# Kernel tuning notes

Measured on AMD Instinct MI355X. Metric: run time of the kernel, lower is better.

Reference implementation:

```python
import jax, jax.numpy as jnp
import numpy as np

T, B, M, H, NH = 4, 8, 1024, 768, 12
HD = H // NH
KMAX = 10


def _ln(x, s, b):
    mu = x.mean(-1, keepdims=True)
    var = ((x - mu) ** 2).mean(-1, keepdims=True)
    return (x - mu) * jax.lax.rsqrt(var + 1e-5) * s + b


def setup_inputs() -> dict:
    key = jax.random.key(0)
    ks = jax.random.split(key, 10)
    init = lambda k, shp: jax.random.normal(k, shp, jnp.float32) * 0.02
    return {
        'x': jax.random.normal(ks[0], (B, M, H), jnp.float32),
        'overlap': jax.random.randint(ks[1], (B, M, M), 0, KMAX + 1, jnp.int32),
        'lp': -jax.random.uniform(ks[2], (B, M), jnp.float32) * 10.0,
        'ln1_s': jnp.ones((T, H)), 'ln1_b': jnp.zeros((T, H)),
        'Wqkv': init(ks[3], (T, H, 3 * H)),
        'Wout': init(ks[4], (T, H, H)), 'bout': jnp.zeros((T, H)),
        'ln2_s': jnp.ones((T, H)), 'ln2_b': jnp.zeros((T, H)),
        'W1': init(ks[5], (T, H, 4 * H)), 'b1': jnp.zeros((T, 4 * H)),
        'W2': init(ks[6], (T, 4 * H, H)), 'b2': jnp.zeros((T, H)),
        'lno_s': jnp.ones((H,)), 'lno_b': jnp.zeros((H,)),
        'ov_emb': init(ks[7], (KMAX + 1,)),
        'ht_alpha': jnp.ones((1,), jnp.float32),
    }


def reference(x, overlap, lp, ln1_s, ln1_b, Wqkv, Wout, bout, ln2_s, ln2_b,
              W1, b1, W2, b2, lno_s, lno_b, ov_emb, ht_alpha):
    lp_c = jnp.clip(lp, -30.0, 0.0)                      # [B,M]
    ov = ov_emb[jnp.minimum(overlap, KMAX)]              # [B,M,M]
    bias = (ov - ht_alpha[0] * lp_c[:, None, :])[:, None]  # [B,1,M,M]
    scale = 1.0 / jnp.sqrt(jnp.float32(HD))
    for t in range(T):
        r = _ln(x, ln1_s[t], ln1_b[t])
        q, k, v = jnp.split(r @ Wqkv[t], 3, axis=-1)
        q = q.reshape(B, M, NH, HD).transpose(0, 2, 1, 3)
        k = k.reshape(B, M, NH, HD).transpose(0, 2, 1, 3)
        v = v.reshape(B, M, NH, HD).transpose(0, 2, 1, 3)
        s = jnp.einsum('bhqd,bhkd->bhqk', q, k) * scale + bias
        a = jax.nn.softmax(s, axis=-1)
        o = jnp.einsum('bhqk,bhkd->bhqd', a, v).transpose(0, 2, 1, 3).reshape(B, M, H)
        x = x + o @ Wout[t] + bout[t]
        h = _ln(x, ln2_s[t], ln2_b[t])
        x = x + jax.nn.gelu(h @ W1[t] + b1[t], approximate=False) @ W2[t] + b2[t]
    x = _ln(x, lno_s, lno_b)
    w = jax.nn.softmax(-lp_c, axis=1)                    # HT weights over m tokens
    return jnp.einsum('bm,bmh->bh', w, x)
```

## Files before the change

### kernel.cpp

```cpp
#include <hip/hip_runtime.h>
#include <hip/hip_bf16.h>
#include <math.h>

#define TT 4
#define BB 8
#define MM 1024
#define HH 768
#define NHEAD 12
#define HDIM 64
#define NTOK 8192
#define H3 2304
#define H4 3072

typedef __attribute__((ext_vector_type(8))) short bf16x8;
typedef __attribute__((ext_vector_type(4))) float f32x4;
typedef __attribute__((ext_vector_type(4))) unsigned short u16x4;

#define GLOBAL_AS(p) ((const __attribute__((address_space(1))) void*)(p))
#define LDS_AS(p)    ((__attribute__((address_space(3))) void*)(p))

__device__ __forceinline__ unsigned short f2bf(float f) {
  union { float f; unsigned u; } v; v.f = f;
  unsigned r = v.u + 0x7fffu + ((v.u >> 16) & 1u);
  return (unsigned short)(r >> 16);
}

__device__ __forceinline__ float fast_exp2(float x) {
#if __has_builtin(__builtin_amdgcn_exp2f)
  return __builtin_amdgcn_exp2f(x);
#else
  return exp2f(x);
#endif
}

__device__ __forceinline__ f32x4 mfma16(bf16x8 a, bf16x8 b, f32x4 c) {
  return __builtin_amdgcn_mfma_f32_16x16x32_bf16(a, b, c, 0, 0, 0);
}

__device__ __forceinline__ float block_sum256(float v, float* sh) {
  #pragma unroll
  for (int off = 32; off > 0; off >>= 1) v += __shfl_down(v, off);
  if ((threadIdx.x & 63) == 0) sh[threadIdx.x >> 6] = v;
  __syncthreads();
  v = sh[0] + sh[1] + sh[2] + sh[3];
  __syncthreads();
  return v;
}

__device__ __forceinline__ float block_max256(float v, float* sh) {
  #pragma unroll
  for (int off = 32; off > 0; off >>= 1) v = fmaxf(v, __shfl_down(v, off));
  if ((threadIdx.x & 63) == 0) sh[threadIdx.x >> 6] = v;
  __syncthreads();
  v = fmaxf(fmaxf(sh[0], sh[1]), fmaxf(sh[2], sh[3]));
  __syncthreads();
  return v;
}

__global__ __launch_bounds__(256) void wconv_kernel(const float* __restrict__ W,
                                                    unsigned short* __restrict__ Wt,
                                                    int K, int N) {
  __shared__ float tile[32][33];
  const int n0 = blockIdx.x * 32, k0 = blockIdx.y * 32;
  const int tx = threadIdx.x, ty = threadIdx.y;
  #pragma unroll
  for (int j = 0; j < 4; j++)
    tile[ty + j*8][tx] = W[(size_t)(k0 + ty + j*8) * N + n0 + tx];
  __syncthreads();
  #pragma unroll
  for (int j = 0; j < 4; j++)
    Wt[(size_t)(n0 + ty + j*8) * K + k0 + tx] = f2bf(tile[tx][ty + j*8]);
}

__global__ __launch_bounds__(256) void ln_kernel(const float* __restrict__ x,
                                                 const float* __restrict__ s,
                                                 const float* __restrict__ b,
                                                 unsigned short* __restrict__ out) {
  __shared__ float sh[4];
  const int row = blockIdx.x;
  const int tid = threadIdx.x;
  const float* xr = x + (size_t)row * HH;
  float v[3];
  float sum = 0.f;
  #pragma unroll
  for (int j = 0; j < 3; j++) { v[j] = xr[tid + j*256]; sum += v[j]; }
  sum = block_sum256(sum, sh);
  const float mu = sum * (1.f/768.f);
  float ss = 0.f;
  #pragma unroll
  for (int j = 0; j < 3; j++) { float d = v[j] - mu; ss += d*d; }
  ss = block_sum256(ss, sh);
  const float rstd = rsqrtf(ss * (1.f/768.f) + 1e-5f);
  #pragma unroll
  for (int j = 0; j < 3; j++) {
    int col = tid + j*256;
    out[(size_t)row * HH + col] = f2bf((v[j]-mu)*rstd*s[col] + b[col]);
  }
}

template<int EPI>
__global__ __launch_bounds__(256) void gemm_kernel(const unsigned short* __restrict__ A,
                                                   const unsigned short* __restrict__ Bt,
                                                   unsigned short* __restrict__ outB,
                                                   float* __restrict__ outF,
                                                   const float* __restrict__ bias,
                                                   int Ng, int Kg, int nx) {
  __shared__ unsigned short a_lds[2][128*64];
  __shared__ unsigned short b_lds[2][128*64];
  const int tid = threadIdx.x;
  const int w = tid >> 6, l = tid & 63;
  const int nwg = gridDim.x;
  const int lin = blockIdx.x;
  const int L = (lin & 7) * (nwg >> 3) + (lin >> 3);
  const int m0 = (L / nx) * 128, n0 = (L % nx) * 128;

  const int wr = (w >> 1) * 64, wc = (w & 1) * 64;
  const int l15 = l & 15, lhi = l >> 4;
  const int srow = w*32 + (l >> 3);
  const int schunk = (l & 7) ^ (l >> 3);
  const int scol = schunk << 3;

  f32x4 acc[4][4] = {};
  const int nk = Kg >> 6;
  int cur = 0;

  #pragma unroll
  for (int i = 0; i < 4; i++) {
    const unsigned short* gsa = A  + (size_t)(m0 + srow + i*8)*Kg + scol;
    const unsigned short* gsb = Bt + (size_t)(n0 + srow + i*8)*Kg + scol;
    __builtin_amdgcn_global_load_lds(GLOBAL_AS(gsa), LDS_AS(&a_lds[0][w*2048 + i*512]), 16, 0, 0);
    __builtin_amdgcn_global_load_lds(GLOBAL_AS(gsb), LDS_AS(&b_lds[0][w*2048 + i*512]), 16, 0, 0);
  }
  __syncthreads();

  for (int t = 0; t < nk; t++) {
    if (t + 1 < nk) {
      const int ks = (t + 1) << 6;
      #pragma unroll
      for (int i = 0; i < 4; i++) {
        const unsigned short* gsa = A  + (size_t)(m0 + srow + i*8)*Kg + ks + scol;
        const unsigned short* gsb = Bt + (size_t)(n0 + srow + i*8)*Kg + ks + scol;
        __builtin_amdgcn_global_load_lds(GLOBAL_AS(gsa), LDS_AS(&a_lds[cur^1][w*2048 + i*512]), 16, 0, 0);
        __builtin_amdgcn_global_load_lds(GLOBAL_AS(gsb), LDS_AS(&b_lds[cur^1][w*2048 + i*512]), 16, 0, 0);
      }
    }
    const unsigned short* ab = &a_lds[cur][0];
    const unsigned short* bb = &b_lds[cur][0];
    #pragma unroll
    for (int kb = 0; kb < 2; kb++) {
      bf16x8 af[4], bfr[4];
      const int rc = (kb*4 + lhi) ^ (l15 & 7);
      #pragma unroll
      for (int rb = 0; rb < 4; rb++)
        af[rb] = *(const bf16x8*)&ab[(wr + rb*16 + l15)*64 + (rc << 3)];
      #pragma unroll
      for (int nb = 0; nb < 4; nb++)
        bfr[nb] = *(const bf16x8*)&bb[(wc + nb*16 + l15)*64 + (rc << 3)];
      #pragma unroll
      for (int rb = 0; rb < 4; rb++)
        #pragma unroll
        for (int nb = 0; nb < 4; nb++)
          acc[rb][nb] = mfma16(af[rb], bfr[nb], acc[rb][nb]);
    }
    __syncthreads();
    cur ^= 1;
  }

  const int lr = lhi << 2;
  #pragma unroll
  for (int rb = 0; rb < 4; rb++)
    #pragma unroll
    for (int nb = 0; nb < 4; nb++) {
      const int row = m0 + wr + rb*16 + lr;
      const int col = n0 + wc + nb*16 + l15;
      #pragma unroll
      for (int r = 0; r < 4; r++) {
        float v = acc[rb][nb][r];
        const size_t off = (size_t)(row + r)*Ng + col;
        if (EPI == 0) {
          outB[off] = f2bf(v);
        } else if (EPI == 1) {
          v += bias[col];
          float u = 0.79788456080287f * v * (1.f + 0.044715f * v * v);
          u = fminf(u, 15.f);
          float e = fast_exp2(u * 2.88539008177793f);
          float th = 1.f - 2.f / (e + 1.f);
          v = 0.5f * v * (1.f + th);
          outB[off] = f2bf(v);
        } else {
          v += bias[col] + outF[off];
          outF[off] = v;
        }
      }
    }
}

__global__ __launch_bounds__(256) void biasprep_kernel(const int* __restrict__ overlap,
                                                       const float* __restrict__ lp,
                                                       const float* __restrict__ ov_emb,
                                                       const float* __restrict__ ht_alpha,
                                                       float* __restrict__ biasP) {
  __shared__ float oe[11];
  if (threadIdx.x < 11) oe[threadIdx.x] = ov_emb[threadIdx.x] * 1.44269504088896f;
  __syncthreads();
  const float aL = ht_alpha[0] * 1.44269504088896f;
  const size_t base = ((size_t)blockIdx.x * 256 + threadIdx.x) * 4;
  const int b = (int)(base >> 20);
  const int k0 = (int)(base & 1023);
  int4 ov = *(const int4*)&overlap[base];
  float4 lv = *(const float4*)&lp[b * MM + k0];
  float4 o4;
  {
    int t0 = ov.x < 10 ? ov.x : 10; float c0 = fminf(fmaxf(lv.x, -30.f), 0.f); o4.x = oe[t0] - aL*c0;
    int t1 = ov.y < 10 ? ov.y : 10; float c1 = fminf(fmaxf(lv.y, -30.f), 0.f); o4.y = oe[t1] - aL*c1;
    int t2 = ov.z < 10 ? ov.z : 10; float c2 = fminf(fmaxf(lv.z, -30.f), 0.f); o4.z = oe[t2] - aL*c2;
    int t3 = ov.w < 10 ? ov.w : 10; float c3 = fminf(fmaxf(lv.w, -30.f), 0.f); o4.w = oe[t3] - aL*c3;
  }
  *(float4*)&biasP[base] = o4;
}

__global__ __launch_bounds__(256) void attn_kernel(const unsigned short* __restrict__ qkv,
                                                   const float* __restrict__ biasP,
                                                   unsigned short* __restrict__ obuf) {
  __shared__ unsigned short k_lds[2][64*64];
  __shared__ unsigned short v_lds[2][64*64];
  __shared__ unsigned short pmat[4][32*64];

  const int tid = threadIdx.x;
  const int w = tid >> 6, l = tid & 63;
  const int lin = blockIdx.x;
  const int L = (lin & 7) * 96 + (lin >> 3);
  const int h = L % 12;
  const int qb = (L / 12) & 7;
  const int b = L / 96;
  const int q0w = qb*128 + w*32;
  const int l15 = l & 15, lhi = l >> 4;
  const float SC = 0.125f * 1.44269504088896f;

  const int kr_s = l >> 3;
  const int schunk = (l & 7) ^ kr_s;
  const int dc = (l & 7) << 3;

  bf16x8 qf[2][2];
  #pragma unroll
  for (int rb = 0; rb < 2; rb++)
    #pragma unroll
    for (int kb = 0; kb < 2; kb++)
      qf[rb][kb] = *(const bf16x8*)&qkv[(size_t)(b*MM + q0w + rb*16 + l15)*H3 + h*HDIM + kb*32 + lhi*8];

  const float* brow[2];
  #pragma unroll
  for (int rb = 0; rb < 2; rb++)
    brow[rb] = biasP + (size_t)(b*MM + q0w + rb*16 + l15) * MM;

  f32x4 oacc[4][2] = {};
  float mrow[2] = {-INFINITY, -INFINITY};
  float lrow[2] = {0.f, 0.f};


  {
    #pragma unroll
    for (int i = 0; i < 2; i++) {
      const unsigned short* g = qkv + (size_t)(b*MM + 0 + i*32 + w*8 + kr_s)*H3 + h*HDIM + HH + schunk*8;
      __builtin_amdgcn_global_load_lds(GLOBAL_AS(g), LDS_AS(&k_lds[0][(i*32 + w*8)*64]), 16, 0, 0);
    }
    bf16x8 vr[2];
    #pragma unroll
    for (int i = 0; i < 2; i++)
      vr[i] = *(const bf16x8*)&qkv[(size_t)(b*MM + 0 + i*32 + w*8 + kr_s)*H3 + h*HDIM + 2*HH + dc];
    #pragma unroll
    for (int i = 0; i < 2; i++) {
      int kr = i*32 + w*8 + kr_s;
      #pragma unroll
      for (int j = 0; j < 8; j++) {
        int key = ((((dc >> 3) & 7) ^ j) & 7) << 3;
        v_lds[0][(dc + j)*64 + (kr ^ key)] = (unsigned short)(short)vr[i][j];
      }
    }
    __syncthreads();
  }

  int cur = 0;
  for (int kt = 0; kt < 16; kt++) {
    const int kbase = kt * 64;
    bf16x8 vrN[2];
    if (kt < 15) {
      const int nbase = kbase + 64;
      #pragma unroll
      for (int i = 0; i < 2; i++) {
        const unsigned short* g = qkv + (size_t)(b*MM + nbase + i*32 + w*8 + kr_s)*H3 + h*HDIM + HH + schunk*8;
        __builtin_amdgcn_global_load_lds(GLOBAL_AS(g), LDS_AS(&k_lds[cur^1][(i*32 + w*8)*64]), 16, 0, 0);
      }
      #pragma unroll
      for (int i = 0; i < 2; i++)
        vrN[i] = *(const bf16x8*)&qkv[(size_t)(b*MM + nbase + i*32 + w*8 + kr_s)*H3 + h*HDIM + 2*HH + dc];
    }

    f32x4 sacc[4][2] = {};
    const unsigned short* kb_lds = &k_lds[cur][0];
    __builtin_amdgcn_s_setprio(1);
    #pragma unroll
    for (int kb = 0; kb < 2; kb++) {
      bf16x8 ak[4];
      #pragma unroll
      for (int nb = 0; nb < 4; nb++) {
        int n = nb*16 + l15;
        ak[nb] = *(const bf16x8*)&kb_lds[n*64 + ((kb*32 + lhi*8) ^ ((n & 7) << 3))];
      }
      #pragma unroll
      for (int nb = 0; nb < 4; nb++)
        #pragma unroll
        for (int rb = 0; rb < 2; rb++)
          sacc[nb][rb] = mfma16(ak[nb], qf[rb][kb], sacc[nb][rb]);
    }
    __builtin_amdgcn_s_setprio(0);

    #pragma unroll
    for (int nb = 0; nb < 4; nb++)
      #pragma unroll
      for (int rb = 0; rb < 2; rb++) {
        f32x4 b4 = *(const f32x4*)&brow[rb][kbase + nb*16 + lhi*4];
        #pragma unroll
        for (int r = 0; r < 4; r++)
          sacc[nb][rb][r] = fmaf(sacc[nb][rb][r], SC, b4[r]);
      }

    float corrf[2];
    int defer[2];
    #pragma unroll
    for (int rb = 0; rb < 2; rb++) {
      float pm = sacc[0][rb][0];
      #pragma unroll
      for (int nb = 0; nb < 4; nb++)
        #pragma unroll
        for (int r = 0; r < 4; r++)
          pm = fmaxf(pm, sacc[nb][rb][r]);
      pm = fmaxf(pm, __shfl_xor(pm, 16));
      pm = fmaxf(pm, __shfl_xor(pm, 32));
      defer[rb] = __all(pm - mrow[rb] <= 8.0f);
      const float mnew = defer[rb] ? mrow[rb] : fmaxf(mrow[rb], pm);
      const float corr = defer[rb] ? 1.0f : fast_exp2(mrow[rb] - mnew);
      float rs = 0.f;
      #pragma unroll
      for (int nb = 0; nb < 4; nb++)
        #pragma unroll
        for (int r = 0; r < 4; r++) {
          float p = fast_exp2(sacc[nb][rb][r] - mnew);
          sacc[nb][rb][r] = p;
          rs += p;
        }
      rs += __shfl_xor(rs, 16);
      rs += __shfl_xor(rs, 32);
      mrow[rb] = mnew;
      lrow[rb] = lrow[rb]*corr + rs;
      corrf[rb] = corr;
    }
    #pragma unroll
    for (int rb = 0; rb < 2; rb++)
      if (!defer[rb]) {
        #pragma unroll
        for (int db = 0; db < 4; db++)
          #pragma unroll
          for (int r = 0; r < 4; r++)
            oacc[db][rb][r] *= corrf[rb];
      }

    unsigned short* pw = &pmat[w][0];
    #pragma unroll
    for (int nb = 0; nb < 4; nb++)
      #pragma unroll
      for (int rb = 0; rb < 2; rb++) {
        u16x4 pk;
        #pragma unroll
        for (int r = 0; r < 4; r++) pk[r] = f2bf(sacc[nb][rb][r]);
        *(u16x4*)&pw[(rb*16 + l15)*64 + ((nb*16 + lhi*4) ^ ((l15 & 7) << 3))] = pk;
      }

    const unsigned short* vb_lds = &v_lds[cur][0];
    __builtin_amdgcn_s_setprio(1);
    #pragma unroll
    for (int kb = 0; kb < 2; kb++) {
      bf16x8 pb[2];
      #pragma unroll
      for (int rb = 0; rb < 2; rb++)
        pb[rb] = *(const bf16x8*)&pw[(rb*16 + l15)*64 + ((kb*32 + lhi*8) ^ ((l15 & 7) << 3))];
      bf16x8 av[4];
      #pragma unroll
      for (int db = 0; db < 4; db++) {
        int d = db*16 + l15;
        int key = ((((d >> 3) & 7) ^ (d & 7)) & 7) << 3;
        av[db] = *(const bf16x8*)&vb_lds[d*64 + ((kb*32 + lhi*8) ^ key)];
      }
      #pragma unroll
      for (int db = 0; db < 4; db++)
        #pragma unroll
        for (int rb = 0; rb < 2; rb++)
          oacc[db][rb] = mfma16(av[db], pb[rb], oacc[db][rb]);
    }
    __builtin_amdgcn_s_setprio(0);

    __syncthreads();
    if (kt < 15) {
      #pragma unroll
      for (int i = 0; i < 2; i++) {
        int kr = i*32 + w*8 + kr_s;
        #pragma unroll
        for (int j = 0; j < 8; j++) {
          int key = ((((dc >> 3) & 7) ^ j) & 7) << 3;
          v_lds[cur^1][(dc + j)*64 + (kr ^ key)] = (unsigned short)(short)vrN[i][j];
        }
      }
    }
    __syncthreads();
    cur ^= 1;
  }

  float inv[2] = { 1.f / lrow[0], 1.f / lrow[1] };
  unsigned short* pw = &pmat[w][0];
  #pragma unroll
  for (int db = 0; db < 4; db++)
    #pragma unroll
    for (int rb = 0; rb < 2; rb++) {
      u16x4 pk;
      #pragma unroll
      for (int r = 0; r < 4; r++) pk[r] = f2bf(oacc[db][rb][r] * inv[rb]);
      *(u16x4*)&pw[(rb*16 + l15)*64 + ((db*16 + lhi*4) ^ ((l15 & 7) << 3))] = pk;
    }
  #pragma unroll
  for (int rep = 0; rep < 4; rep++) {
    int qq = rep*8 + (l >> 3);
    int d0 = (l & 7) << 3;
    bf16x8 vv = *(const bf16x8*)&pw[qq*64 + (d0 ^ ((qq & 7) << 3))];
    *(bf16x8*)&obuf[(size_t)(b*MM + q0w + qq)*HH + h*HDIM + d0] = vv;
  }
}

__global__ __launch_bounds__(256) void htw_kernel(const float* __restrict__ lp,
                                                  float* __restrict__ w_ht) {
  __shared__ float sh[4];
  const int b = blockIdx.x, tid = threadIdx.x;
  float vals[4];
  float mx = -INFINITY;
  #pragma unroll
  for (int j = 0; j < 4; j++) {
    float lv = lp[b*MM + tid + j*256];
    float lc = fminf(fmaxf(lv, -30.f), 0.f);
    vals[j] = -lc;
    mx = fmaxf(mx, vals[j]);
  }
  mx = block_max256(mx, sh);
  float se = 0.f;
  #pragma unroll
  for (int j = 0; j < 4; j++) { vals[j] = expf(vals[j] - mx); se += vals[j]; }
  se = block_sum256(se, sh);
  const float inv = 1.f / se;
  #pragma unroll
  for (int j = 0; j < 4; j++) w_ht[b*MM + tid + j*256] = vals[j] * inv;
}

__global__ __launch_bounds__(256) void final_partial_kernel(const float* __restrict__ xbuf,
                                                            const float* __restrict__ lno_s,
                                                            const float* __restrict__ lno_b,
                                                            const float* __restrict__ w_ht,
                                                            float* __restrict__ part) {
  __shared__ float sh[4];
  const int b = blockIdx.x >> 4;
  const int chunk = blockIdx.x & 15;
  const int tid = threadIdx.x;
  float acc[3] = {0.f, 0.f, 0.f};
  float sc[3], bc[3];
  #pragma unroll
  for (int j = 0; j < 3; j++) { sc[j] = lno_s[tid + j*256]; bc[j] = lno_b[tid + j*256]; }
  for (int rr = 0; rr < 64; rr++) {
    const int tok = b*MM + chunk*64 + rr;
    const float* xr = xbuf + (size_t)tok * HH;
    float v[3]; float sum = 0.f;
    #pragma unroll
    for (int j = 0; j < 3; j++) { v[j] = xr[tid + j*256]; sum += v[j]; }
    sum = block_sum256(sum, sh);
    const float mu = sum * (1.f/768.f);
    float ss = 0.f;
    #pragma unroll
    for (int j = 0; j < 3; j++) { float d = v[j] - mu; ss += d*d; }
    ss = block_sum256(ss, sh);
    const float rstd = rsqrtf(ss * (1.f/768.f) + 1e-5f);
    const float wgt = w_ht[b*MM + chunk*64 + rr];
    #pragma unroll
    for (int j = 0; j < 3; j++) acc[j] += wgt * ((v[j]-mu)*rstd*sc[j] + bc[j]);
  }
  #pragma unroll
  for (int j = 0; j < 3; j++) part[(size_t)blockIdx.x * HH + tid + j*256] = acc[j];
}

__global__ __launch_bounds__(256) void final_reduce_kernel(const float* __restrict__ part,
                                                           float* __restrict__ out) {
  const int b = blockIdx.x;
  const int col = blockIdx.y*256 + threadIdx.x;
  float s = 0.f;
  #pragma unroll
  for (int c = 0; c < 16; c++) s += part[(size_t)(b*16 + c) * HH + col];
  out[b*HH + col] = s;
}

extern "C" void kernel_launch(void* const* d_in, const int* in_sizes, int n_in,
                              void* d_out, int out_size, void* d_ws, size_t ws_size,
                              hipStream_t stream) {
  (void)in_sizes; (void)n_in;
  const float* x      = (const float*)d_in[0];
  const int*   overlap= (const int*)d_in[1];
  const float* lp     = (const float*)d_in[2];
  const float* ln1_s  = (const float*)d_in[3];
  const float* ln1_b  = (const float*)d_in[4];
  const float* Wqkv   = (const float*)d_in[5];
  const float* Wout   = (const float*)d_in[6];
  const float* bout   = (const float*)d_in[7];
  const float* ln2_s  = (const float*)d_in[8];
  const float* ln2_b  = (const float*)d_in[9];
  const float* W1     = (const float*)d_in[10];
  const float* b1     = (const float*)d_in[11];
  const float* W2     = (const float*)d_in[12];
  const float* b2     = (const float*)d_in[13];
  const float* lno_s  = (const float*)d_in[14];
  const float* lno_b  = (const float*)d_in[15];
  const float* ov_emb = (const float*)d_in[16];
  const float* ht_alpha = (const float*)d_in[17];
  float* out = (float*)d_out;

  char* ws = (char*)d_ws;
  float*          xbuf  = (float*)(ws + 0);
  unsigned short* lnout = (unsigned short*)(ws + 25165824);
  unsigned short* qkv   = (unsigned short*)(ws + 37748736);
  unsigned short* obuf  = (unsigned short*)(ws + 75497472);
  unsigned short* gbuf  = (unsigned short*)(ws + 88080384);
  unsigned short* wbuf  = (unsigned short*)(ws + 138412032);
  float*          w_ht  = (float*)(ws + 143130624);
  float*          part  = (float*)(ws + 143163392);
  const int prep_once = (ws_size >= (size_t)143556608 + (size_t)33554432);
  float*          biasP = prep_once ? (float*)(ws + 143556608) : (float*)gbuf;

  hipMemcpyAsync(xbuf, x, (size_t)NTOK * HH * sizeof(float), hipMemcpyDeviceToDevice, stream);
  htw_kernel<<<BB, 256, 0, stream>>>(lp, w_ht);
  if (prep_once)
    biasprep_kernel<<<(BB*MM*MM/4)/256, 256, 0, stream>>>(overlap, lp, ov_emb, ht_alpha, biasP);

  for (int t = 0; t < TT; t++) {
    wconv_kernel<<<dim3(H3/32, HH/32), dim3(32, 8), 0, stream>>>(Wqkv + (size_t)t*HH*H3, wbuf, HH, H3);
    ln_kernel<<<NTOK, 256, 0, stream>>>(xbuf, ln1_s + t*HH, ln1_b + t*HH, lnout);
    gemm_kernel<0><<<(H3/128)*(NTOK/128), 256, 0, stream>>>(lnout, wbuf, qkv, nullptr, nullptr, H3, HH, H3/128);
    if (!prep_once)
      biasprep_kernel<<<(BB*MM*MM/4)/256, 256, 0, stream>>>(overlap, lp, ov_emb, ht_alpha, biasP);
    attn_kernel<<<BB*NHEAD*(MM/128), 256, 0, stream>>>(qkv, biasP, obuf);
    wconv_kernel<<<dim3(HH/32, HH/32), dim3(32, 8), 0, stream>>>(Wout + (size_t)t*HH*HH, wbuf, HH, HH);
    gemm_kernel<2><<<(HH/128)*(NTOK/128), 256, 0, stream>>>(obuf, wbuf, nullptr, xbuf, bout + t*HH, HH, HH, HH/128);
    ln_kernel<<<NTOK, 256, 0, stream>>>(xbuf, ln2_s + t*HH, ln2_b + t*HH, lnout);
    wconv_kernel<<<dim3(H4/32, HH/32), dim3(32, 8), 0, stream>>>(W1 + (size_t)t*HH*H4, wbuf, HH, H4);
    gemm_kernel<1><<<(H4/128)*(NTOK/128), 256, 0, stream>>>(lnout, wbuf, gbuf, nullptr, b1 + t*H4, H4, HH, H4/128);
    wconv_kernel<<<dim3(HH/32, H4/32), dim3(32, 8), 0, stream>>>(W2 + (size_t)t*H4*HH, wbuf, H4, HH);
    gemm_kernel<2><<<(HH/128)*(NTOK/128), 256, 0, stream>>>(gbuf, wbuf, nullptr, xbuf, b2 + t*HH, HH, H4, HH/128);
  }

  final_partial_kernel<<<BB*16, 256, 0, stream>>>(xbuf, lno_s, lno_b, w_ht, part);
  final_reduce_kernel<<<dim3(BB, 3), 256, 0, stream>>>(part, out);

  (void)out_size;
}
```

Baseline: 1.443 ms.

## Restructure attention K/V pipeline to one barrier per tile, prefetch bias, use packed bf16 convert

The attention kernel now fetches V two tiles ahead into registers and writes it to the alternate LDS buffer at the top of each iteration. This removes the second __syncthreads per key tile. Bias values are loaded into registers before the QK MFMAs so their global latency overlaps the compute. The manual bf16 rounding is replaced with the v_cvt_pk_bf16_f32 instruction, which cuts VALU work. In exchange it uses more registers, and the correctness of the buffer reuse now rests on the single remaining barrier.

```diff
diff --git a/kernel.cpp b/kernel.cpp
--- a/kernel.cpp
+++ b/kernel.cpp
@@ -23,6 +23,12 @@
   union { float f; unsigned u; } v; v.f = f;
   unsigned r = v.u + 0x7fffu + ((v.u >> 16) & 1u);
   return (unsigned short)(r >> 16);
+}
+
+__device__ __forceinline__ unsigned cvt_pk_bf16(float lo, float hi) {
+  unsigned r;
+  asm("v_cvt_pk_bf16_f32 %0, %1, %2" : "=v"(r) : "v"(lo), "v"(hi));
+  return r;
 }
 
 __device__ __forceinline__ float fast_exp2(float x) {
@@ -257,17 +263,17 @@
   float mrow[2] = {-INFINITY, -INFINITY};
   float lrow[2] = {0.f, 0.f};
 
-
+  bf16x8 vcur[2];
   {
     #pragma unroll
     for (int i = 0; i < 2; i++) {
-      const unsigned short* g = qkv + (size_t)(b*MM + 0 + i*32 + w*8 + kr_s)*H3 + h*HDIM + HH + schunk*8;
+      const unsigned short* g = qkv + (size_t)(b*MM + i*32 + w*8 + kr_s)*H3 + h*HDIM + HH + schunk*8;
       __builtin_amdgcn_global_load_lds(GLOBAL_AS(g), LDS_AS(&k_lds[0][(i*32 + w*8)*64]), 16, 0, 0);
     }
     bf16x8 vr[2];
     #pragma unroll
     for (int i = 0; i < 2; i++)
-      vr[i] = *(const bf16x8*)&qkv[(size_t)(b*MM + 0 + i*32 + w*8 + kr_s)*H3 + h*HDIM + 2*HH + dc];
+      vr[i] = *(const bf16x8*)&qkv[(size_t)(b*MM + i*32 + w*8 + kr_s)*H3 + h*HDIM + 2*HH + dc];
     #pragma unroll
     for (int i = 0; i < 2; i++) {
       int kr = i*32 + w*8 + kr_s;
@@ -277,24 +283,45 @@
         v_lds[0][(dc + j)*64 + (kr ^ key)] = (unsigned short)(short)vr[i][j];
       }
     }
+    #pragma unroll
+    for (int i = 0; i < 2; i++)
+      vcur[i] = *(const bf16x8*)&qkv[(size_t)(b*MM + 64 + i*32 + w*8 + kr_s)*H3 + h*HDIM + 2*HH + dc];
     __syncthreads();
   }
 
-  int cur = 0;
   for (int kt = 0; kt < 16; kt++) {
+    const int cur = kt & 1;
     const int kbase = kt * 64;
-    bf16x8 vrN[2];
+
     if (kt < 15) {
+      #pragma unroll
+      for (int i = 0; i < 2; i++) {
+        int kr = i*32 + w*8 + kr_s;
+        #pragma unroll
+        for (int j = 0; j < 8; j++) {
+          int key = ((((dc >> 3) & 7) ^ j) & 7) << 3;
+          v_lds[cur^1][(dc + j)*64 + (kr ^ key)] = (unsigned short)(short)vcur[i][j];
+        }
+      }
       const int nbase = kbase + 64;
       #pragma unroll
       for (int i = 0; i < 2; i++) {
         const unsigned short* g = qkv + (size_t)(b*MM + nbase + i*32 + w*8 + kr_s)*H3 + h*HDIM + HH + schunk*8;
         __builtin_amdgcn_global_load_lds(GLOBAL_AS(g), LDS_AS(&k_lds[cur^1][(i*32 + w*8)*64]), 16, 0, 0);
       }
+    }
+    if (kt < 14) {
+      const int n2 = kbase + 128;
       #pragma unroll
       for (int i = 0; i < 2; i++)
-        vrN[i] = *(const bf16x8*)&qkv[(size_t)(b*MM + nbase + i*32 + w*8 + kr_s)*H3 + h*HDIM + 2*HH + dc];
-    }
+        vcur[i] = *(const bf16x8*)&qkv[(size_t)(b*MM + n2 + i*32 + w*8 + kr_s)*H3 + h*HDIM + 2*HH + dc];
+    }
+    f32x4 bregs[4][2];
+    #pragma unroll
+    for (int nb = 0; nb < 4; nb++)
+      #pragma unroll
+      for (int rb = 0; rb < 2; rb++)
+        bregs[nb][rb] = *(const f32x4*)&brow[rb][kbase + nb*16 + lhi*4];
 
     f32x4 sacc[4][2] = {};
     const unsigned short* kb_lds = &k_lds[cur][0];
@@ -318,12 +345,10 @@
     #pragma unroll
     for (int nb = 0; nb < 4; nb++)
       #pragma unroll
-      for (int rb = 0; rb < 2; rb++) {
-        f32x4 b4 = *(const f32x4*)&brow[rb][kbase + nb*16 + lhi*4];
+      for (int rb = 0; rb < 2; rb++)
         #pragma unroll
         for (int r = 0; r < 4; r++)
-          sacc[nb][rb][r] = fmaf(sacc[nb][rb][r], SC, b4[r]);
-      }
+          sacc[nb][rb][r] = fmaf(sacc[nb][rb][r], SC, bregs[nb][rb][r]);
 
     float corrf[2];
     int defer[2];
@@ -370,10 +395,10 @@
     for (int nb = 0; nb < 4; nb++)
       #pragma unroll
       for (int rb = 0; rb < 2; rb++) {
-        u16x4 pk;
-        #pragma unroll
-        for (int r = 0; r < 4; r++) pk[r] = f2bf(sacc[nb][rb][r]);
-        *(u16x4*)&pw[(rb*16 + l15)*64 + ((nb*16 + lhi*4) ^ ((l15 & 7) << 3))] = pk;
+        uint2 pk;
+        pk.x = cvt_pk_bf16(sacc[nb][rb][0], sacc[nb][rb][1]);
+        pk.y = cvt_pk_bf16(sacc[nb][rb][2], sacc[nb][rb][3]);
+        *(uint2*)&pw[(rb*16 + l15)*64 + ((nb*16 + lhi*4) ^ ((l15 & 7) << 3))] = pk;
       }
 
     const unsigned short* vb_lds = &v_lds[cur][0];
@@ -400,19 +425,6 @@
     __builtin_amdgcn_s_setprio(0);
 
     __syncthreads();
-    if (kt < 15) {
-      #pragma unroll
-      for (int i = 0; i < 2; i++) {
-        int kr = i*32 + w*8 + kr_s;
-        #pragma unroll
-        for (int j = 0; j < 8; j++) {
-          int key = ((((dc >> 3) & 7) ^ j) & 7) << 3;
-          v_lds[cur^1][(dc + j)*64 + (kr ^ key)] = (unsigned short)(short)vrN[i][j];
-        }
-      }
-    }
-    __syncthreads();
-    cur ^= 1;
   }
 
   float inv[2] = { 1.f / lrow[0], 1.f / lrow[1] };
@@ -421,10 +433,10 @@
   for (int db = 0; db < 4; db++)
     #pragma unroll
     for (int rb = 0; rb < 2; rb++) {
-      u16x4 pk;
-      #pragma unroll
-      for (int r = 0; r < 4; r++) pk[r] = f2bf(oacc[db][rb][r] * inv[rb]);
-      *(u16x4*)&pw[(rb*16 + l15)*64 + ((db*16 + lhi*4) ^ ((l15 & 7) << 3))] = pk;
+      uint2 pk;
+      pk.x = cvt_pk_bf16(oacc[db][rb][0] * inv[rb], oacc[db][rb][1] * inv[rb]);
+      pk.y = cvt_pk_bf16(oacc[db][rb][2] * inv[rb], oacc[db][rb][3] * inv[rb]);
+      *(uint2*)&pw[(rb*16 + l15)*64 + ((db*16 + lhi*4) ^ ((l15 & 7) << 3))] = pk;
     }
   #pragma unroll
   for (int rep = 0; rep < 4; rep++) {
```

New measurement: 1.397 ms. 3.2% less time.
